# Kernel tuning notes

Measured on AMD Instinct MI355X. Metric: run time of the kernel, lower is better.

Reference implementation:

```python
import jax, jax.numpy as jnp
import numpy as np

EPS = 1e-06

def _mlp(x, Ws):
    # chained Linear(bias=False) + ReLU, applied per depth layer
    for i in range(Ws.shape[0]):
        x = jax.nn.relu(x @ Ws[i].T)  # torch Linear: x @ W^T
    return x

def setup_inputs() -> dict:
    key = jax.random.key(0)
    k1, k2, k3 = jax.random.split(key, 3)
    B, N, D, depth = 4, 4096, 64, 2
    x = jax.random.normal(k1, (B, N, D), dtype=jnp.float32)
    # kaiming-uniform-ish init scale for Linear(64,64)
    s = 1.0 / np.sqrt(D)
    W_enc = jax.random.uniform(k2, (depth, D, D), dtype=jnp.float32, minval=-s, maxval=s)
    W_dec = jax.random.uniform(k3, (depth, D, D), dtype=jnp.float32, minval=-s, maxval=s)
    return {"x": x, "W_enc": W_enc, "W_dec": W_dec}

def reference(x, W_enc, W_dec):
    y = _mlp(x, W_enc)                                   # [B,N,D]
    y = y / (jnp.linalg.norm(y, axis=-1, keepdims=True) + EPS)
    cmp_matrix = jnp.einsum('bnd,bmd->bnm', y, y)        # [B,N,N] (no softmax)
    y = jnp.einsum('bnm,bmd->bnd', cmp_matrix, y)        # [B,N,D]
    return _mlp(y, W_dec)
```

## Files before the change

kernel.cpp:

```cpp
#include <hip/hip_runtime.h>


typedef _Float16 h8 __attribute__((ext_vector_type(8)));
typedef float    f4 __attribute__((ext_vector_type(4)));
typedef unsigned long long u64;

constexpr unsigned KEY = 0xD7A5C3F1u;

#define RFL(v) __builtin_amdgcn_readfirstlane(v)

__device__ __forceinline__ u64 ic_load64(const u64* p) {
    return __hip_atomic_load(p, __ATOMIC_RELAXED, __HIP_MEMORY_SCOPE_AGENT);
}
__device__ __forceinline__ void ic_store64(u64* p, u64 v) {
    __hip_atomic_store(p, v, __ATOMIC_RELAXED, __HIP_MEMORY_SCOPE_AGENT);
}
__device__ __forceinline__ void ic_store_u(unsigned* p, unsigned v) {
    __hip_atomic_store(p, v, __ATOMIC_RELAXED, __HIP_MEMORY_SCOPE_AGENT);
}
__device__ __forceinline__ unsigned ic_load_u(const unsigned* p) {
    return __hip_atomic_load(p, __ATOMIC_RELAXED, __HIP_MEMORY_SCOPE_AGENT);
}

__device__ __forceinline__ f4 mfma16(h8 a, h8 b, f4 c) {
    return __builtin_amdgcn_mfma_f32_16x16x32_f16(a, b, c, 0, 0, 0);
}
__device__ __forceinline__ h8 mkfrag_f32(const float* p) {
    const float4 a = *(const float4*)p;
    const float4 b = *(const float4*)(p + 4);
    h8 r;
    r[0]=(_Float16)a.x; r[1]=(_Float16)a.y; r[2]=(_Float16)a.z; r[3]=(_Float16)a.w;
    r[4]=(_Float16)b.x; r[5]=(_Float16)b.y; r[6]=(_Float16)b.z; r[7]=(_Float16)b.w;
    return r;
}

union HU { _Float16 h; unsigned short u; };
union PK { u64 v; unsigned short u[4]; };

__global__ __launch_bounds__(512) void fused(
        const float* __restrict__ x,
        const float* __restrict__ We,
        const float* __restrict__ Wd,
        float* __restrict__ out,
        u64* __restrict__ partGu,
        u64* __restrict__ Gu,
        unsigned* __restrict__ flagP,
        unsigned* __restrict__ flagG) {
    __shared__ __align__(16) float sT [32][68];
    __shared__ __align__(16) float sTt[64][36];
    __shared__ __align__(16) float sGf[64][68];
    __shared__ __align__(16) float4 sRed[64][4];
    __shared__ __align__(16) float sSS[32][4];
    __shared__ float sScale[32];

    const int t = threadIdx.x;
    const int l = t & 63, c = l & 15, g = l >> 4;
    const int w = RFL(t >> 6), ti = w >> 2, tj = w & 3;
    const int blk = blockIdx.x, bb = blk >> 7;
    const long base = (long)blk * 2048;

    h8 wE0[2], wE1[2], wD0[2], wD1[2];
#pragma unroll
    for (int kh = 0; kh < 2; ++kh) {
        const int n = tj * 16 + c;
        wE0[kh] = mkfrag_f32(We +        n * 64 + kh * 32 + g * 8);
        wE1[kh] = mkfrag_f32(We + 4096 + n * 64 + kh * 32 + g * 8);
        wD0[kh] = mkfrag_f32(Wd +        n * 64 + kh * 32 + g * 8);
        wD1[kh] = mkfrag_f32(Wd + 4096 + n * 64 + kh * 32 + g * 8);
    }

    {
        const float4 v = ((const float4*)(x + base))[t];
        *(float4*)&sT[t >> 4][(t & 15) * 4] = v;
    }
    __syncthreads();

    auto rowfragT = [&](int row, int kh) -> h8 {
        return mkfrag_f32(&sT[row][kh * 32 + g * 8]);
    };

    f4 d = {0.f, 0.f, 0.f, 0.f};
#pragma unroll
    for (int kh = 0; kh < 2; ++kh) d = mfma16(rowfragT(16*ti + c, kh), wE0[kh], d);
    __syncthreads();
#pragma unroll
    for (int i = 0; i < 4; ++i) sT[16*ti + 4*g + i][16*tj + c] = fmaxf(d[i], 0.f);
    __syncthreads();

    d = (f4){0.f, 0.f, 0.f, 0.f};
#pragma unroll
    for (int kh = 0; kh < 2; ++kh) d = mfma16(rowfragT(16*ti + c, kh), wE1[kh], d);
    float hv[4];
#pragma unroll
    for (int i = 0; i < 4; ++i) hv[i] = fmaxf(d[i], 0.f);

    float sq[4];
#pragma unroll
    for (int i = 0; i < 4; ++i) sq[i] = hv[i] * hv[i];
#pragma unroll
    for (int m = 1; m < 16; m <<= 1) {
#pragma unroll
        for (int i = 0; i < 4; ++i) sq[i] += __shfl_xor(sq[i], m);
    }
    if (c == 0) {
#pragma unroll
        for (int i = 0; i < 4; ++i) sSS[16*ti + 4*g + i][tj] = sq[i];
    }
    __syncthreads();
    if (t < 32) {
        const float4 s4 = *(const float4*)&sSS[t][0];
        sScale[t] = 1.f / (sqrtf(s4.x + s4.y + s4.z + s4.w) + 1e-6f);
    }
    __syncthreads();

    {
        float yv4[4];
#pragma unroll
        for (int i = 0; i < 4; ++i) {
            const int row = 16*ti + 4*g + i;
            yv4[i] = hv[i] * sScale[row];
            sT[row][16*tj + c] = yv4[i];
        }
        *(float4*)&sTt[16*tj + c][16*ti + 4*g] =
            make_float4(yv4[0], yv4[1], yv4[2], yv4[3]);
    }
    __syncthreads();

    {
        const h8 fB  = mkfrag_f32(&sTt[16*tj + c][g * 8]);
        const h8 fA0 = mkfrag_f32(&sTt[16*ti + c][g * 8]);
        const h8 fA1 = mkfrag_f32(&sTt[16*(ti + 2) + c][g * 8]);
        const f4 z4 = {0.f, 0.f, 0.f, 0.f};
        const f4 ga0 = mfma16(fA0, fB, z4);
        const f4 ga1 = mfma16(fA1, fB, z4);
        PK o0, o1;
#pragma unroll
        for (int i = 0; i < 4; ++i) {
            HU a; a.h = (_Float16)ga0[i]; o0.u[i] = a.u;
            HU b; b.h = (_Float16)ga1[i]; o1.u[i] = b.u;
        }
        ic_store64(&partGu[(long)blk * 1024 + 2 * t],     o0.v);
        ic_store64(&partGu[(long)blk * 1024 + 2 * t + 1], o1.v);
    }

    asm volatile("s_waitcnt vmcnt(0)" ::: "memory");
    __syncthreads();
    if (t == 0) ic_store_u(&flagP[blk], KEY);

    if (blk < 64) {
        const int rb = blk >> 4, s = blk & 15;
        if (t < 128) {
            unsigned spins = 0;
            while (ic_load_u(&flagP[rb * 128 + t]) != KEY) {
                __builtin_amdgcn_s_sleep(1);
                if (++spins > 30000000u) break;
            }
        }
        __syncthreads();
        if (t < 256) {
            const int slot_l = t & 63, q4 = t >> 6;
            const u64* src = partGu + (long)rb * 128 * 1024 + s * 64 + slot_l;
            float a0 = 0.f, a1 = 0.f, a2 = 0.f, a3 = 0.f;
#pragma unroll 16
            for (int j = q4 * 32; j < q4 * 32 + 32; ++j) {
                PK p; p.v = ic_load64(src + (long)j * 1024);
                HU e0, e1, e2, e3;
                e0.u = p.u[0]; e1.u = p.u[1]; e2.u = p.u[2]; e3.u = p.u[3];
                a0 += (float)e0.h; a1 += (float)e1.h;
                a2 += (float)e2.h; a3 += (float)e3.h;
            }
            sRed[slot_l][q4] = make_float4(a0, a1, a2, a3);
        }
        __syncthreads();
        if (t < 64) {
            const float4 r0 = sRed[t][0], r1 = sRed[t][1];
            const float4 r2 = sRed[t][2], r3 = sRed[t][3];
            const float f0 = ((r0.x + r1.x) + (r2.x + r3.x));
            const float f1 = ((r0.y + r1.y) + (r2.y + r3.y));
            const float f2 = ((r0.z + r1.z) + (r2.z + r3.z));
            const float f3 = ((r0.w + r1.w) + (r2.w + r3.w));
            PK o;
            { HU z; z.h = (_Float16)f0; o.u[0] = z.u; }
            { HU z; z.h = (_Float16)f1; o.u[1] = z.u; }
            { HU z; z.h = (_Float16)f2; o.u[2] = z.u; }
            { HU z; z.h = (_Float16)f3; o.u[3] = z.u; }
            ic_store64(&Gu[rb * 1024 + s * 64 + t], o.v);
            asm volatile("s_waitcnt vmcnt(0)" ::: "memory");
        }
        __syncthreads();
        if (t == 0) ic_store_u(&flagG[rb * 16 + s], KEY);
    }

    if (t < 16) {
        unsigned spins = 0;
        while (ic_load_u(&flagG[bb * 16 + t]) != KEY) {
            __builtin_amdgcn_s_sleep(1);
            if (++spins > 30000000u) break;
        }
    }
    __syncthreads();
    asm volatile("" ::: "memory");

    {
#pragma unroll
        for (int kk = 0; kk < 2; ++kk) {
            const int u = kk * 512 + t;
            PK p; p.v = ic_load64(&Gu[bb * 1024 + u]);
            const int t_src = u >> 1, pp = u & 1;
            const int w_s = t_src >> 6, l_s = t_src & 63;
            const int ti_s = (w_s >> 2) + 2 * pp, tj_s = w_s & 3;
            const int c_s = l_s & 15, g_s = l_s >> 4;
            const int col = 16 * tj_s + c_s;
#pragma unroll
            for (int i = 0; i < 4; ++i) {
                HU a; a.u = p.u[i];
                sGf[16 * ti_s + 4 * g_s + i][col] = (float)a.h;
            }
        }
    }
    __syncthreads();

    f4 z = {0.f, 0.f, 0.f, 0.f};
#pragma unroll
    for (int kh = 0; kh < 2; ++kh)
        z = mfma16(rowfragT(16*ti + c, kh),
                   mkfrag_f32(&sGf[16*tj + c][kh * 32 + g * 8]), z);
    __syncthreads();
#pragma unroll
    for (int i = 0; i < 4; ++i) sT[16*ti + 4*g + i][16*tj + c] = z[i];
    __syncthreads();

    d = (f4){0.f, 0.f, 0.f, 0.f};
#pragma unroll
    for (int kh = 0; kh < 2; ++kh) d = mfma16(rowfragT(16*ti + c, kh), wD0[kh], d);
    __syncthreads();
#pragma unroll
    for (int i = 0; i < 4; ++i) sT[16*ti + 4*g + i][16*tj + c] = fmaxf(d[i], 0.f);
    __syncthreads();

    d = (f4){0.f, 0.f, 0.f, 0.f};
#pragma unroll
    for (int kh = 0; kh < 2; ++kh) d = mfma16(rowfragT(16*ti + c, kh), wD1[kh], d);
#pragma unroll
    for (int i = 0; i < 4; ++i)
        out[base + (16*ti + 4*g + i) * 64 + 16*tj + c] = fmaxf(d[i], 0.f);
}

extern "C" void kernel_launch(void* const* d_in, const int* in_sizes, int n_in,
                              void* d_out, int out_size, void* d_ws, size_t ws_size,
                              hipStream_t stream) {
    const float* x  = (const float*)d_in[0];
    const float* We = (const float*)d_in[1];
    const float* Wd = (const float*)d_in[2];
    float* outp = (float*)d_out;
    char*  ws   = (char*)d_ws;

    u64*      partGu = (u64*)ws;
    u64*      Gu     = partGu + 512 * 1024;
    unsigned* flagP  = (unsigned*)(Gu + 4 * 1024);
    unsigned* flagG  = flagP + 512;

    fused<<<512, 512, 0, stream>>>(x, We, Wd, outp, partGu, Gu, flagP, flagG);
}
```

Baseline: 23.73 us.

## Split work into 1024 blocks of 16 rows and read Gram matrix directly

Halves rows per block (16 instead of 32) and threads per block (256), doubling the grid to 1024 blocks with launch bounds requesting 4 blocks per CU. Each block now writes its 64x64 partial Gram matrix in row-major fp16, staged through shared memory, so the final stage can load Gram fragments straight from global memory instead of unpacking into a float shared buffer. The reduction stage uses 128 reducer blocks, each summing 256 partials. This doubles partial-sum traffic and the number of flags to spin on, in exchange for shorter per-block serial chains and more resident waves.

```diff
diff --git a/kernel.cpp b/kernel.cpp
--- a/kernel.cpp
+++ b/kernel.cpp
@@ -4,8 +4,9 @@
 typedef _Float16 h8 __attribute__((ext_vector_type(8)));
 typedef float    f4 __attribute__((ext_vector_type(4)));
 typedef unsigned long long u64;
-
-constexpr unsigned KEY = 0xD7A5C3F1u;
+typedef unsigned short u16;
+
+constexpr unsigned KEY = 0xE9C7B5A3u;
 
 #define RFL(v) __builtin_amdgcn_readfirstlane(v)
 
@@ -34,10 +35,10 @@
     return r;
 }
 
-union HU { _Float16 h; unsigned short u; };
-union PK { u64 v; unsigned short u[4]; };
-
-__global__ __launch_bounds__(512) void fused(
+union HU { _Float16 h; u16 u; };
+union PK { u64 v; u16 u[4]; };
+
+__global__ __launch_bounds__(256, 4) void fused(
         const float* __restrict__ x,
         const float* __restrict__ We,
         const float* __restrict__ Wd,
@@ -46,23 +47,23 @@
         u64* __restrict__ Gu,
         unsigned* __restrict__ flagP,
         unsigned* __restrict__ flagG) {
-    __shared__ __align__(16) float sT [32][68];
+    __shared__ __align__(16) float sT [16][68];
     __shared__ __align__(16) float sTt[64][36];
-    __shared__ __align__(16) float sGf[64][68];
-    __shared__ __align__(16) float4 sRed[64][4];
-    __shared__ __align__(16) float sSS[32][4];
-    __shared__ float sScale[32];
+    __shared__ __align__(16) u16   sP[4096];
+    __shared__ __align__(16) float4 sRed[32][8];
+    __shared__ __align__(16) float sSS[16][4];
+    __shared__ float sScale[16];
 
     const int t = threadIdx.x;
     const int l = t & 63, c = l & 15, g = l >> 4;
-    const int w = RFL(t >> 6), ti = w >> 2, tj = w & 3;
-    const int blk = blockIdx.x, bb = blk >> 7;
-    const long base = (long)blk * 2048;
+    const int w = RFL(t >> 6);
+    const int blk = blockIdx.x, bb = blk >> 8;
+    const long base = (long)blk * 1024;
 
     h8 wE0[2], wE1[2], wD0[2], wD1[2];
 #pragma unroll
     for (int kh = 0; kh < 2; ++kh) {
-        const int n = tj * 16 + c;
+        const int n = 16 * w + c;
         wE0[kh] = mkfrag_f32(We +        n * 64 + kh * 32 + g * 8);
         wE1[kh] = mkfrag_f32(We + 4096 + n * 64 + kh * 32 + g * 8);
         wD0[kh] = mkfrag_f32(Wd +        n * 64 + kh * 32 + g * 8);
@@ -70,6 +71,8 @@
     }
 
     {
+#pragma unroll
+        for (int i = t; i < 64 * 16; i += 256) sTt[i >> 4][16 + (i & 15)] = 0.f;
         const float4 v = ((const float4*)(x + base))[t];
         *(float4*)&sT[t >> 4][(t & 15) * 4] = v;
     }
@@ -81,15 +84,15 @@
 
     f4 d = {0.f, 0.f, 0.f, 0.f};
 #pragma unroll
-    for (int kh = 0; kh < 2; ++kh) d = mfma16(rowfragT(16*ti + c, kh), wE0[kh], d);
-    __syncthreads();
-#pragma unroll
-    for (int i = 0; i < 4; ++i) sT[16*ti + 4*g + i][16*tj + c] = fmaxf(d[i], 0.f);
+    for (int kh = 0; kh < 2; ++kh) d = mfma16(rowfragT(c, kh), wE0[kh], d);
+    __syncthreads();
+#pragma unroll
+    for (int i = 0; i < 4; ++i) sT[4*g + i][16*w + c] = fmaxf(d[i], 0.f);
     __syncthreads();
 
     d = (f4){0.f, 0.f, 0.f, 0.f};
 #pragma unroll
-    for (int kh = 0; kh < 2; ++kh) d = mfma16(rowfragT(16*ti + c, kh), wE1[kh], d);
+    for (int kh = 0; kh < 2; ++kh) d = mfma16(rowfragT(c, kh), wE1[kh], d);
     float hv[4];
 #pragma unroll
     for (int i = 0; i < 4; ++i) hv[i] = fmaxf(d[i], 0.f);
@@ -104,10 +107,10 @@
     }
     if (c == 0) {
 #pragma unroll
-        for (int i = 0; i < 4; ++i) sSS[16*ti + 4*g + i][tj] = sq[i];
-    }
-    __syncthreads();
-    if (t < 32) {
+        for (int i = 0; i < 4; ++i) sSS[4*g + i][w] = sq[i];
+    }
+    __syncthreads();
+    if (t < 16) {
         const float4 s4 = *(const float4*)&sSS[t][0];
         sScale[t] = 1.f / (sqrtf(s4.x + s4.y + s4.z + s4.w) + 1e-6f);
     }
@@ -117,83 +120,87 @@
         float yv4[4];
 #pragma unroll
         for (int i = 0; i < 4; ++i) {
-            const int row = 16*ti + 4*g + i;
+            const int row = 4*g + i;
             yv4[i] = hv[i] * sScale[row];
-            sT[row][16*tj + c] = yv4[i];
-        }
-        *(float4*)&sTt[16*tj + c][16*ti + 4*g] =
-            make_float4(yv4[0], yv4[1], yv4[2], yv4[3]);
-    }
-    __syncthreads();
-
-    {
-        const h8 fB  = mkfrag_f32(&sTt[16*tj + c][g * 8]);
-        const h8 fA0 = mkfrag_f32(&sTt[16*ti + c][g * 8]);
-        const h8 fA1 = mkfrag_f32(&sTt[16*(ti + 2) + c][g * 8]);
-        const f4 z4 = {0.f, 0.f, 0.f, 0.f};
-        const f4 ga0 = mfma16(fA0, fB, z4);
-        const f4 ga1 = mfma16(fA1, fB, z4);
-        PK o0, o1;
-#pragma unroll
-        for (int i = 0; i < 4; ++i) {
-            HU a; a.h = (_Float16)ga0[i]; o0.u[i] = a.u;
-            HU b; b.h = (_Float16)ga1[i]; o1.u[i] = b.u;
-        }
-        ic_store64(&partGu[(long)blk * 1024 + 2 * t],     o0.v);
-        ic_store64(&partGu[(long)blk * 1024 + 2 * t + 1], o1.v);
+            sT[row][16*w + c] = yv4[i];
+        }
+        *(float4*)&sTt[16*w + c][4*g] = make_float4(yv4[0], yv4[1], yv4[2], yv4[3]);
+    }
+    __syncthreads();
+
+    {
+        const h8 fB = mkfrag_f32(&sTt[16*w + c][g * 8]);
+#pragma unroll
+        for (int ti = 0; ti < 4; ++ti) {
+            const h8 fA = mkfrag_f32(&sTt[16*ti + c][g * 8]);
+            const f4 z4 = {0.f, 0.f, 0.f, 0.f};
+            const f4 ga = mfma16(fA, fB, z4);
+#pragma unroll
+            for (int i = 0; i < 4; ++i) {
+                HU a; a.h = (_Float16)ga[i];
+                sP[(16*ti + 4*g + i) * 64 + 16*w + c] = a.u;
+            }
+        }
+    }
+    __syncthreads();
+    {
+        const u64* sp = (const u64*)&sP[t * 16];
+#pragma unroll
+        for (int k = 0; k < 4; ++k)
+            ic_store64(&partGu[(long)blk * 1024 + t * 4 + k], sp[k]);
     }
 
     asm volatile("s_waitcnt vmcnt(0)" ::: "memory");
     __syncthreads();
     if (t == 0) ic_store_u(&flagP[blk], KEY);
 
-    if (blk < 64) {
-        const int rb = blk >> 4, s = blk & 15;
-        if (t < 128) {
+    if (blk < 128) {
+        const int rb = blk >> 5, s = blk & 31;
+        {
             unsigned spins = 0;
-            while (ic_load_u(&flagP[rb * 128 + t]) != KEY) {
+            while (ic_load_u(&flagP[rb * 256 + t]) != KEY) {
                 __builtin_amdgcn_s_sleep(1);
                 if (++spins > 30000000u) break;
             }
         }
         __syncthreads();
-        if (t < 256) {
-            const int slot_l = t & 63, q4 = t >> 6;
-            const u64* src = partGu + (long)rb * 128 * 1024 + s * 64 + slot_l;
+        {
+            const int slot_l = t & 31, q8 = t >> 5;
+            const u64* src = partGu + (long)rb * 256 * 1024 + s * 32 + slot_l;
             float a0 = 0.f, a1 = 0.f, a2 = 0.f, a3 = 0.f;
 #pragma unroll 16
-            for (int j = q4 * 32; j < q4 * 32 + 32; ++j) {
+            for (int j = q8 * 32; j < q8 * 32 + 32; ++j) {
                 PK p; p.v = ic_load64(src + (long)j * 1024);
                 HU e0, e1, e2, e3;
                 e0.u = p.u[0]; e1.u = p.u[1]; e2.u = p.u[2]; e3.u = p.u[3];
                 a0 += (float)e0.h; a1 += (float)e1.h;
                 a2 += (float)e2.h; a3 += (float)e3.h;
             }
-            sRed[slot_l][q4] = make_float4(a0, a1, a2, a3);
-        }
-        __syncthreads();
-        if (t < 64) {
-            const float4 r0 = sRed[t][0], r1 = sRed[t][1];
-            const float4 r2 = sRed[t][2], r3 = sRed[t][3];
-            const float f0 = ((r0.x + r1.x) + (r2.x + r3.x));
-            const float f1 = ((r0.y + r1.y) + (r2.y + r3.y));
-            const float f2 = ((r0.z + r1.z) + (r2.z + r3.z));
-            const float f3 = ((r0.w + r1.w) + (r2.w + r3.w));
+            sRed[slot_l][q8] = make_float4(a0, a1, a2, a3);
+        }
+        __syncthreads();
+        if (t < 32) {
+            float f0 = 0.f, f1 = 0.f, f2 = 0.f, f3 = 0.f;
+#pragma unroll
+            for (int j = 0; j < 8; ++j) {
+                const float4 r = sRed[t][j];
+                f0 += r.x; f1 += r.y; f2 += r.z; f3 += r.w;
+            }
             PK o;
             { HU z; z.h = (_Float16)f0; o.u[0] = z.u; }
             { HU z; z.h = (_Float16)f1; o.u[1] = z.u; }
             { HU z; z.h = (_Float16)f2; o.u[2] = z.u; }
             { HU z; z.h = (_Float16)f3; o.u[3] = z.u; }
-            ic_store64(&Gu[rb * 1024 + s * 64 + t], o.v);
+            ic_store64(&Gu[rb * 1024 + s * 32 + t], o.v);
             asm volatile("s_waitcnt vmcnt(0)" ::: "memory");
         }
         __syncthreads();
-        if (t == 0) ic_store_u(&flagG[rb * 16 + s], KEY);
-    }
-
-    if (t < 16) {
+        if (t == 0) ic_store_u(&flagG[rb * 32 + s], KEY);
+    }
+
+    if (t < 32) {
         unsigned spins = 0;
-        while (ic_load_u(&flagG[bb * 16 + t]) != KEY) {
+        while (ic_load_u(&flagG[bb * 32 + t]) != KEY) {
             __builtin_amdgcn_s_sleep(1);
             if (++spins > 30000000u) break;
         }
@@ -202,48 +209,33 @@
     asm volatile("" ::: "memory");
 
     {
-#pragma unroll
-        for (int kk = 0; kk < 2; ++kk) {
-            const int u = kk * 512 + t;
-            PK p; p.v = ic_load64(&Gu[bb * 1024 + u]);
-            const int t_src = u >> 1, pp = u & 1;
-            const int w_s = t_src >> 6, l_s = t_src & 63;
-            const int ti_s = (w_s >> 2) + 2 * pp, tj_s = w_s & 3;
-            const int c_s = l_s & 15, g_s = l_s >> 4;
-            const int col = 16 * tj_s + c_s;
-#pragma unroll
-            for (int i = 0; i < 4; ++i) {
-                HU a; a.u = p.u[i];
-                sGf[16 * ti_s + 4 * g_s + i][col] = (float)a.h;
-            }
-        }
-    }
-    __syncthreads();
-
-    f4 z = {0.f, 0.f, 0.f, 0.f};
-#pragma unroll
-    for (int kh = 0; kh < 2; ++kh)
-        z = mfma16(rowfragT(16*ti + c, kh),
-                   mkfrag_f32(&sGf[16*tj + c][kh * 32 + g * 8]), z);
-    __syncthreads();
-#pragma unroll
-    for (int i = 0; i < 4; ++i) sT[16*ti + 4*g + i][16*tj + c] = z[i];
+        const _Float16* Gh = (const _Float16*)Gu + (long)bb * 4096;
+        f4 z = {0.f, 0.f, 0.f, 0.f};
+#pragma unroll
+        for (int kh = 0; kh < 2; ++kh) {
+            const h8 gb = *(const h8*)&Gh[(16*w + c) * 64 + kh * 32 + g * 8];
+            z = mfma16(rowfragT(c, kh), gb, z);
+        }
+        __syncthreads();
+#pragma unroll
+        for (int i = 0; i < 4; ++i) sT[4*g + i][16*w + c] = z[i];
+    }
     __syncthreads();
 
     d = (f4){0.f, 0.f, 0.f, 0.f};
 #pragma unroll
-    for (int kh = 0; kh < 2; ++kh) d = mfma16(rowfragT(16*ti + c, kh), wD0[kh], d);
-    __syncthreads();
-#pragma unroll
-    for (int i = 0; i < 4; ++i) sT[16*ti + 4*g + i][16*tj + c] = fmaxf(d[i], 0.f);
+    for (int kh = 0; kh < 2; ++kh) d = mfma16(rowfragT(c, kh), wD0[kh], d);
+    __syncthreads();
+#pragma unroll
+    for (int i = 0; i < 4; ++i) sT[4*g + i][16*w + c] = fmaxf(d[i], 0.f);
     __syncthreads();
 
     d = (f4){0.f, 0.f, 0.f, 0.f};
 #pragma unroll
-    for (int kh = 0; kh < 2; ++kh) d = mfma16(rowfragT(16*ti + c, kh), wD1[kh], d);
+    for (int kh = 0; kh < 2; ++kh) d = mfma16(rowfragT(c, kh), wD1[kh], d);
 #pragma unroll
     for (int i = 0; i < 4; ++i)
-        out[base + (16*ti + 4*g + i) * 64 + 16*tj + c] = fmaxf(d[i], 0.f);
+        out[base + (4*g + i) * 64 + 16*w + c] = fmaxf(d[i], 0.f);
 }
 
 extern "C" void kernel_launch(void* const* d_in, const int* in_sizes, int n_in,
@@ -256,9 +248,9 @@
     char*  ws   = (char*)d_ws;
 
     u64*      partGu = (u64*)ws;
-    u64*      Gu     = partGu + 512 * 1024;
+    u64*      Gu     = partGu + 1024 * 1024;
     unsigned* flagP  = (unsigned*)(Gu + 4 * 1024);
-    unsigned* flagG  = flagP + 512;
-
-    fused<<<512, 512, 0, stream>>>(x, We, Wd, outp, partGu, Gu, flagP, flagG);
-}
+    unsigned* flagG  = flagP + 1024;
+
+    fused<<<1024, 256, 0, stream>>>(x, We, Wd, outp, partGu, Gu, flagP, flagG);
+}
```

After: 25.85 us. 1.09x slower.

## Ping-pong LDS buffers, inline norm scale, read Gram directly from global in MFMA layout

Applied to the files above, without the earlier changes.

Adds a second shared buffer so consecutive MLP layers alternate between sT and sU, removing one barrier per layer. The per-row norm scale is now computed by each thread from sSS instead of a separate pass with an extra barrier. The reduced Gram matrix is written to global memory in a permuted order that matches the MFMA B-fragment layout, so the final block reads h8 fragments directly rather than staging through LDS. This removes several __syncthreads and an LDS round-trip, at the cost of redundant sqrt work, uncoalesced permuted stores and reads of the Gram tile from global/L2.

```diff
diff --git a/kernel.cpp b/kernel.cpp
--- a/kernel.cpp
+++ b/kernel.cpp
@@ -4,8 +4,9 @@
 typedef _Float16 h8 __attribute__((ext_vector_type(8)));
 typedef float    f4 __attribute__((ext_vector_type(4)));
 typedef unsigned long long u64;
-
-constexpr unsigned KEY = 0xD7A5C3F1u;
+typedef unsigned short u16;
+
+constexpr unsigned KEY = 0xF1B39D57u;
 
 #define RFL(v) __builtin_amdgcn_readfirstlane(v)
 
@@ -34,8 +35,17 @@
     return r;
 }
 
-union HU { _Float16 h; unsigned short u; };
-union PK { u64 v; unsigned short u[4]; };
+union HU { _Float16 h; u16 u; };
+union PK { u64 v; u16 u[4]; };
+
+__device__ __forceinline__ int permG(int u) {
+    const int p  = u & 1;
+    const int c  = (u >> 1) & 15;
+    const int g  = (u >> 5) & 3;
+    const int wv = (u >> 7) & 7;
+    const int TI = (wv >> 2) + 2 * p, tj = wv & 3;
+    return (16 * tj + c) * 16 + 4 * TI + g;
+}
 
 __global__ __launch_bounds__(512) void fused(
         const float* __restrict__ x,
@@ -47,11 +57,10 @@
         unsigned* __restrict__ flagP,
         unsigned* __restrict__ flagG) {
     __shared__ __align__(16) float sT [32][68];
+    __shared__ __align__(16) float sU [32][68];
     __shared__ __align__(16) float sTt[64][36];
-    __shared__ __align__(16) float sGf[64][68];
     __shared__ __align__(16) float4 sRed[64][4];
     __shared__ __align__(16) float sSS[32][4];
-    __shared__ float sScale[32];
 
     const int t = threadIdx.x;
     const int l = t & 63, c = l & 15, g = l >> 4;
@@ -75,21 +84,19 @@
     }
     __syncthreads();
 
-    auto rowfragT = [&](int row, int kh) -> h8 {
-        return mkfrag_f32(&sT[row][kh * 32 + g * 8]);
-    };
+    auto fragT = [&](int row, int kh) -> h8 { return mkfrag_f32(&sT[row][kh*32 + g*8]); };
+    auto fragU = [&](int row, int kh) -> h8 { return mkfrag_f32(&sU[row][kh*32 + g*8]); };
 
     f4 d = {0.f, 0.f, 0.f, 0.f};
 #pragma unroll
-    for (int kh = 0; kh < 2; ++kh) d = mfma16(rowfragT(16*ti + c, kh), wE0[kh], d);
-    __syncthreads();
-#pragma unroll
-    for (int i = 0; i < 4; ++i) sT[16*ti + 4*g + i][16*tj + c] = fmaxf(d[i], 0.f);
+    for (int kh = 0; kh < 2; ++kh) d = mfma16(fragT(16*ti + c, kh), wE0[kh], d);
+#pragma unroll
+    for (int i = 0; i < 4; ++i) sU[16*ti + 4*g + i][16*tj + c] = fmaxf(d[i], 0.f);
     __syncthreads();
 
     d = (f4){0.f, 0.f, 0.f, 0.f};
 #pragma unroll
-    for (int kh = 0; kh < 2; ++kh) d = mfma16(rowfragT(16*ti + c, kh), wE1[kh], d);
+    for (int kh = 0; kh < 2; ++kh) d = mfma16(fragU(16*ti + c, kh), wE1[kh], d);
     float hv[4];
 #pragma unroll
     for (int i = 0; i < 4; ++i) hv[i] = fmaxf(d[i], 0.f);
@@ -105,11 +112,6 @@
     if (c == 0) {
 #pragma unroll
         for (int i = 0; i < 4; ++i) sSS[16*ti + 4*g + i][tj] = sq[i];
-    }
-    __syncthreads();
-    if (t < 32) {
-        const float4 s4 = *(const float4*)&sSS[t][0];
-        sScale[t] = 1.f / (sqrtf(s4.x + s4.y + s4.z + s4.w) + 1e-6f);
     }
     __syncthreads();
 
@@ -118,7 +120,9 @@
 #pragma unroll
         for (int i = 0; i < 4; ++i) {
             const int row = 16*ti + 4*g + i;
-            yv4[i] = hv[i] * sScale[row];
+            const float4 s4 = *(const float4*)&sSS[row][0];
+            const float scale = 1.f / (sqrtf(s4.x + s4.y + s4.z + s4.w) + 1e-6f);
+            yv4[i] = hv[i] * scale;
             sT[row][16*tj + c] = yv4[i];
         }
         *(float4*)&sTt[16*tj + c][16*ti + 4*g] =
@@ -184,7 +188,7 @@
             { HU z; z.h = (_Float16)f1; o.u[1] = z.u; }
             { HU z; z.h = (_Float16)f2; o.u[2] = z.u; }
             { HU z; z.h = (_Float16)f3; o.u[3] = z.u; }
-            ic_store64(&Gu[rb * 1024 + s * 64 + t], o.v);
+            ic_store64(&Gu[rb * 1024 + permG(s * 64 + t)], o.v);
             asm volatile("s_waitcnt vmcnt(0)" ::: "memory");
         }
         __syncthreads();
@@ -202,45 +206,28 @@
     asm volatile("" ::: "memory");
 
     {
-#pragma unroll
-        for (int kk = 0; kk < 2; ++kk) {
-            const int u = kk * 512 + t;
-            PK p; p.v = ic_load64(&Gu[bb * 1024 + u]);
-            const int t_src = u >> 1, pp = u & 1;
-            const int w_s = t_src >> 6, l_s = t_src & 63;
-            const int ti_s = (w_s >> 2) + 2 * pp, tj_s = w_s & 3;
-            const int c_s = l_s & 15, g_s = l_s >> 4;
-            const int col = 16 * tj_s + c_s;
-#pragma unroll
-            for (int i = 0; i < 4; ++i) {
-                HU a; a.u = p.u[i];
-                sGf[16 * ti_s + 4 * g_s + i][col] = (float)a.h;
-            }
-        }
-    }
-    __syncthreads();
-
-    f4 z = {0.f, 0.f, 0.f, 0.f};
-#pragma unroll
-    for (int kh = 0; kh < 2; ++kh)
-        z = mfma16(rowfragT(16*ti + c, kh),
-                   mkfrag_f32(&sGf[16*tj + c][kh * 32 + g * 8]), z);
-    __syncthreads();
-#pragma unroll
-    for (int i = 0; i < 4; ++i) sT[16*ti + 4*g + i][16*tj + c] = z[i];
+        const _Float16* Gh = (const _Float16*)Gu + (long)bb * 4096;
+        f4 z = {0.f, 0.f, 0.f, 0.f};
+#pragma unroll
+        for (int kh = 0; kh < 2; ++kh) {
+            const h8 gb = *(const h8*)&Gh[(16*tj + c) * 64 + kh * 32 + g * 8];
+            z = mfma16(fragT(16*ti + c, kh), gb, z);
+        }
+#pragma unroll
+        for (int i = 0; i < 4; ++i) sU[16*ti + 4*g + i][16*tj + c] = z[i];
+    }
     __syncthreads();
 
     d = (f4){0.f, 0.f, 0.f, 0.f};
 #pragma unroll
-    for (int kh = 0; kh < 2; ++kh) d = mfma16(rowfragT(16*ti + c, kh), wD0[kh], d);
-    __syncthreads();
+    for (int kh = 0; kh < 2; ++kh) d = mfma16(fragU(16*ti + c, kh), wD0[kh], d);
 #pragma unroll
     for (int i = 0; i < 4; ++i) sT[16*ti + 4*g + i][16*tj + c] = fmaxf(d[i], 0.f);
     __syncthreads();
 
     d = (f4){0.f, 0.f, 0.f, 0.f};
 #pragma unroll
-    for (int kh = 0; kh < 2; ++kh) d = mfma16(rowfragT(16*ti + c, kh), wD1[kh], d);
+    for (int kh = 0; kh < 2; ++kh) d = mfma16(fragT(16*ti + c, kh), wD1[kh], d);
 #pragma unroll
     for (int i = 0; i < 4; ++i)
         out[base + (16*ti + 4*g + i) * 64 + 16*tj + c] = fmaxf(d[i], 0.f);
```

Measured after the change: 22.07 us, median of 2. 7.0% less time.
